# Optimization experiments

Hardware: AMD Instinct MI355X
Metric: run time of the kernel (lower is better)

The kernel has to match this reference:

```python
import jax, jax.numpy as jnp
import numpy as np

DEPTH = 16
Q_DIM = 64
V_DIM = 64
BATCH = 2048


def setup_inputs() -> dict:
    key = jax.random.key(0)
    k1, k2, k3 = jax.random.split(key, 3)
    query = jax.random.normal(k1, (BATCH, Q_DIM), dtype=jnp.float32)
    # internal-node keys: (2^depth - 1) nodes, each with 2 child keys of dim q_dim
    tree_key = jax.random.normal(k2, (2 ** DEPTH - 1, 2, Q_DIM), dtype=jnp.float32)
    # leaf values: 2^depth leaves of dim v_dim
    tree_value = jax.random.normal(k3, (2 ** DEPTH, V_DIM), dtype=jnp.float32)
    return {"query": query, "tree_key": tree_key, "tree_value": tree_value}


def _tree_attention(query, tree_key, tree_value, depth):
    # Hierarchical softmax attention over a complete binary tree.
    # At each internal node, a 2-way softmax over <query, child_key> logits
    # splits probability mass between left/right subtrees; leaf weight is the
    # product of probabilities along its root-to-leaf path.
    B = query.shape[0]
    probs = jnp.ones((B, 1), dtype=query.dtype)
    start = 0
    for d in range(depth):
        n = 2 ** d  # nodes at this level, stored contiguously at [start, start+n)
        level_keys = tree_key[start:start + n]           # (n, 2, q_dim)
        logits = jnp.einsum('bq,ncq->bnc', query, level_keys)  # (B, n, 2)
        p = jax.nn.softmax(logits, axis=-1)               # (B, n, 2)
        probs = (probs[:, :, None] * p).reshape(B, 2 * n)  # (B, 2n)
        start += n
    # weighted combination of leaf values: (B, 2^depth) @ (2^depth, v_dim)
    return probs @ tree_value


def reference(query, tree_key, tree_value):
    return _tree_attention(query, tree_key, tree_value, DEPTH)
```

## Files before the change

kernel.cpp:

```cpp
#include <hip/hip_runtime.h>

#define LOG2E 1.44269504088896f

typedef _Float16 half8  __attribute__((ext_vector_type(8)));
typedef _Float16 half4v __attribute__((ext_vector_type(4)));
typedef float    floatx4 __attribute__((ext_vector_type(4)));

#define WS_KD   0u
#define WS_VT   8388608u
#define WS_PART 16777216u

__device__ __forceinline__ floatx4 mfma16(half8 a, half8 b, floatx4 c) {
    return __builtin_amdgcn_mfma_f32_16x16x32_f16(a, b, c, 0, 0, 0);
}

__device__ __forceinline__ float sigmf(float d) {
    return __builtin_amdgcn_rcpf(1.0f + __builtin_amdgcn_exp2f(d * (-LOG2E)));
}

__device__ __forceinline__ void gl_lds16(const void* gsrc, void* ldst) {
    __builtin_amdgcn_global_load_lds(
        (const __attribute__((address_space(1))) unsigned int*)gsrc,
        (__attribute__((address_space(3))) unsigned int*)ldst,
        16, 0, 0);
}

__global__ __launch_bounds__(256)
void prep_kd(const float* __restrict__ tkey, char* __restrict__ ws)
{
    const int gt  = blockIdx.x * 256 + threadIdx.x;
    const int rid = gt >> 3, part = gt & 7;
    const int s = rid >> 6, j = rid & 63;
    const size_t dst = (size_t)WS_KD + (size_t)s * 8192 + j * 128 + ((part * 16) ^ ((j & 7) << 4));
    half8 out;
    if (j < 63) {
        const int u = j + 1;
        const int f = 31 - __builtin_clz(u);
        const int i = u - (1 << f);
        const int gidx = ((1 << (10 + f)) - 1) + (s << f) + i;
        const floatx4* kp = (const floatx4*)(tkey + (size_t)gidx * 128) + part * 2;
        floatx4 a0 = kp[0], a1 = kp[1];
        floatx4 b0 = kp[16], b1 = kp[17];
        #pragma unroll
        for (int e = 0; e < 4; ++e) {
            out[e]     = (_Float16)(a0[e] - b0[e]);
            out[4 + e] = (_Float16)(a1[e] - b1[e]);
        }
    } else {
        #pragma unroll
        for (int e = 0; e < 8; ++e) out[e] = (_Float16)0.f;
    }
    *(half8*)(ws + dst) = out;
}

__global__ __launch_bounds__(256)
void prep_vt(const float* __restrict__ tval, char* __restrict__ ws)
{
    __shared__ _Float16 sT[64 * 72];
    const int s = blockIdx.x, tid = threadIdx.x;
    {
        const int l = tid >> 2, part = tid & 3;
        const floatx4* vp = (const floatx4*)(tval + ((size_t)s * 64 + l) * 64) + part * 4;
        #pragma unroll
        for (int t4 = 0; t4 < 4; ++t4) {
            floatx4 f = vp[t4];
            #pragma unroll
            for (int e = 0; e < 4; ++e)
                sT[(part * 16 + t4 * 4 + e) * 72 + l] = (_Float16)f[e];
        }
    }
    __syncthreads();
    {
        const int v = tid >> 2, q4 = tid & 3;
        half8 x0 = *(const half8*)(sT + v * 72 + 16 * q4);
        half8 x1 = *(const half8*)(sT + v * 72 + 16 * q4 + 8);
        char* base = ws + WS_VT + (size_t)s * 8192 + v * 128;
        const int swz = (v & 7) << 4;
        *(half8*)(base + ((q4 * 32)      ^ swz)) = x0;
        *(half8*)(base + ((q4 * 32 + 16) ^ swz)) = x1;
    }
}

#define RD(n) ((float)sProb[(n) * 256 + (bb ^ (((n) & 7) << 3))])

__global__ __launch_bounds__(256, 2)
void tree_attn(const float* __restrict__ q,
               const float* __restrict__ tkey,
               const char* __restrict__ wsc,
               _Float16* __restrict__ pout)
{
    __shared__ _Float16 sA[256 * 72];
    __shared__ _Float16 sProb[64 * 256];
    __shared__ _Float16 sB[64 * 64];

    const int tid  = threadIdx.x;
    const int w    = tid >> 6;
    const int lane = tid & 63;
    const int lm   = lane & 15;
    const int quad = lane >> 4;
    const int xcd  = blockIdx.x & 7;
    const int ix   = blockIdx.x >> 3;
    const int g    = xcd * 8 + (ix >> 3);
    const int tb   = ix & 7;

    {
        const int j = tid >> 3, part = tid & 7;
        int gidx = -1;
        if (j < 6) {
            gidx = (1 << j) - 1 + (g >> (6 - j));
        } else if (j < 21) {
            const int u = j - 5;
            const int e = 31 - __builtin_clz(u);
            const int i = u - (1 << e);
            gidx = ((1 << (6 + e)) - 1) + (g << e) + i;
        }
        half8 out;
        if (gidx >= 0) {
            const floatx4* kp = (const floatx4*)(tkey + (size_t)gidx * 128) + part * 2;
            floatx4 a0 = kp[0], a1 = kp[1];
            floatx4 b0 = kp[16], b1 = kp[17];
            #pragma unroll
            for (int e = 0; e < 4; ++e) {
                out[e]     = (_Float16)(a0[e] - b0[e]);
                out[4 + e] = (_Float16)(a1[e] - b1[e]);
            }
        } else {
            #pragma unroll
            for (int e = 0; e < 8; ++e) out[e] = (_Float16)0.f;
        }
        *(half8*)(sB + j * 64 + ((part * 8) ^ ((j & 7) << 3))) = out;
    }

    {
        const int r = tid;
        const floatx4* qp = (const floatx4*)(q + (size_t)(tb * 256 + r) * 64);
        const int sw = (r & 7) << 3;
        #pragma unroll
        for (int t4 = 0; t4 < 8; ++t4) {
            floatx4 f0 = qp[2 * t4], f1 = qp[2 * t4 + 1];
            half8 hv;
            #pragma unroll
            for (int e = 0; e < 4; ++e) { hv[e] = (_Float16)f0[e]; hv[4 + e] = (_Float16)f1[e]; }
            *(half8*)(sA + r * 64 + ((t4 * 8) ^ sw)) = hv;
        }
    }
    __syncthreads();

    half8 qA[4][2];
    #pragma unroll
    for (int m = 0; m < 4; ++m) {
        const int rA = 64 * w + 16 * m + lm;
        const int sw = (lm & 7) << 3;
        #pragma unroll
        for (int kt = 0; kt < 2; ++kt)
            qA[m][kt] = *(const half8*)(sA + rA * 64 + ((kt * 32 + quad * 8) ^ sw));
    }

    {
        #pragma unroll
        for (int nt = 0; nt < 2; ++nt) {
            const int row = 16 * nt + lm;
            const int sw = (lm & 7) << 3;
            half8 bf0 = *(const half8*)(sB + row * 64 + ((quad * 8) ^ sw));
            half8 bf1 = *(const half8*)(sB + row * 64 + ((32 + quad * 8) ^ sw));
            floatx4 acc[4];
            #pragma unroll
            for (int m = 0; m < 4; ++m) {
                acc[m][0] = 0.f; acc[m][1] = 0.f; acc[m][2] = 0.f; acc[m][3] = 0.f;
                acc[m] = mfma16(qA[m][0], bf0, acc[m]);
                acc[m] = mfma16(qA[m][1], bf1, acc[m]);
            }
            #pragma unroll
            for (int m = 0; m < 4; ++m) {
                half4v ph;
                #pragma unroll
                for (int r = 0; r < 4; ++r) ph[r] = (_Float16)sigmf(acc[m][r]);
                const int col = 64 * w + 16 * m + 4 * quad;
                *(half4v*)(sProb + row * 256 + (col ^ sw)) = ph;
            }
        }
    }
    __syncthreads();

    const int bb = tid;
    float pref = 1.f;
    #pragma unroll
    for (int d = 0; d < 6; ++d) {
        float pv = RD(d);
        pref *= ((g >> (5 - d)) & 1) ? (1.f - pv) : pv;
    }
    const float p6   = RD(6);
    const float p7_0 = RD(7),  p7_1 = RD(8);
    const float p9_0 = RD(9),  p9_1 = RD(10), p9_2 = RD(11), p9_3 = RD(12);
    const float p13_0 = RD(13), p13_1 = RD(14), p13_2 = RD(15), p13_3 = RD(16);
    const float p13_4 = RD(17), p13_5 = RD(18), p13_6 = RD(19), p13_7 = RD(20);

    floatx4 O[4][4];
    #pragma unroll
    for (int m = 0; m < 4; ++m)
        #pragma unroll
        for (int nt = 0; nt < 4; ++nt) { O[m][nt][0]=0.f; O[m][nt][1]=0.f; O[m][nt][2]=0.f; O[m][nt][3]=0.f; }

    for (int sl = 0; sl < 16; ++sl) {
        const int s = (g << 4) + sl;

        {
            const char* kd = wsc + WS_KD + (size_t)s * 8192;
            gl_lds16(kd + w * 2048 +        lane * 16, sB + w * 1024);
            gl_lds16(kd + w * 2048 + 1024 + lane * 16, sB + w * 1024 + 512);
        }
        half8 vf[4][2];
        {
            const char* vt = wsc + WS_VT + (size_t)s * 8192;
            #pragma unroll
            for (int nt = 0; nt < 4; ++nt) {
                const int row = 16 * nt + lm;
                const int swz = (lm & 7) << 4;
                #pragma unroll
                for (int kt = 0; kt < 2; ++kt)
                    vf[nt][kt] = *(const half8*)(vt + row * 128 + ((kt * 64 + quad * 16) ^ swz));
            }
        }
        __syncthreads();

        __builtin_amdgcn_s_setprio(1);
        #pragma unroll
        for (int nt = 0; nt < 4; ++nt) {
            const int row = 16 * nt + lm;
            const int sw = (lm & 7) << 3;
            half8 bf0 = *(const half8*)(sB + row * 64 + ((quad * 8) ^ sw));
            half8 bf1 = *(const half8*)(sB + row * 64 + ((32 + quad * 8) ^ sw));
            floatx4 acc[4];
            #pragma unroll
            for (int m = 0; m < 4; ++m) {
                acc[m][0] = 0.f; acc[m][1] = 0.f; acc[m][2] = 0.f; acc[m][3] = 0.f;
                acc[m] = mfma16(qA[m][0], bf0, acc[m]);
                acc[m] = mfma16(qA[m][1], bf1, acc[m]);
            }
            #pragma unroll
            for (int m = 0; m < 4; ++m) {
                half4v ph;
                #pragma unroll
                for (int r = 0; r < 4; ++r) ph[r] = (_Float16)sigmf(acc[m][r]);
                const int col = 64 * w + 16 * m + 4 * quad;
                *(half4v*)(sProb + row * 256 + (col ^ sw)) = ph;
            }
        }
        __builtin_amdgcn_s_setprio(0);
        __syncthreads();

        const int a0 = sl >> 3, a1 = sl >> 2, a2 = sl >> 1;
        float P0v = pref * (a0 ? (1.f - p6) : p6);
        { float v7 = a0 ? p7_1 : p7_0;                    P0v *= (a1 & 1) ? (1.f - v7) : v7; }
        { float v9 = (a1 == 0) ? p9_0 : (a1 == 1) ? p9_1 : (a1 == 2) ? p9_2 : p9_3;
                                                          P0v *= (a2 & 1) ? (1.f - v9) : v9; }
        { float vd = (a2 == 0) ? p13_0 : (a2 == 1) ? p13_1 : (a2 == 2) ? p13_2 : (a2 == 3) ? p13_3
                   : (a2 == 4) ? p13_4 : (a2 == 5) ? p13_5 : (a2 == 6) ? p13_6 : p13_7;
                                                          P0v *= (sl & 1) ? (1.f - vd) : vd; }

        {
            #pragma unroll
            for (int qq = 0; qq < 4; ++qq) {
                float p0 = RD(0);
                float p1 = RD(1 + (qq >> 1));
                float P2 = P0v * (((qq >> 1) & 1) ? (1.f - p0) : p0)
                               * ((qq & 1) ? (1.f - p1) : p1);
                float p2 = RD(3 + qq);
                float A3[2]; A3[0] = P2 * p2; A3[1] = P2 * (1.f - p2);
                float A4[4];
                #pragma unroll
                for (int c = 0; c < 2; ++c) {
                    float pv = RD(7 + 2 * qq + c);
                    A4[2 * c] = A3[c] * pv; A4[2 * c + 1] = A3[c] * (1.f - pv);
                }
                float A5[8];
                #pragma unroll
                for (int n = 0; n < 4; ++n) {
                    float pv = RD(15 + 4 * qq + n);
                    A5[2 * n] = A4[n] * pv; A5[2 * n + 1] = A4[n] * (1.f - pv);
                }
                half8 lo, hi;
                #pragma unroll
                for (int n = 0; n < 8; ++n) {
                    float pv = RD(31 + 8 * qq + n);
                    float e0 = A5[n] * pv;
                    float e1 = A5[n] * (1.f - pv);
                    if (n < 4) { lo[2 * n] = (_Float16)e0; lo[2 * n + 1] = (_Float16)e1; }
                    else       { hi[2 * (n - 4)] = (_Float16)e0; hi[2 * (n - 4) + 1] = (_Float16)e1; }
                }
                const int sw = (bb & 7) << 3;
                *(half8*)(sA + bb * 64 + ((16 * qq)     ^ sw)) = lo;
                *(half8*)(sA + bb * 64 + ((16 * qq + 8) ^ sw)) = hi;
            }
        }
        __syncthreads();

        {
            half8 af[4][2];
            #pragma unroll
            for (int m = 0; m < 4; ++m) {
                const int rA = 64 * w + 16 * m + lm;
                const int sw = (lm & 7) << 3;
                #pragma unroll
                for (int kt = 0; kt < 2; ++kt)
                    af[m][kt] = *(const half8*)(sA + rA * 64 + ((kt * 32 + quad * 8) ^ sw));
            }
            __builtin_amdgcn_s_setprio(1);
            #pragma unroll
            for (int nt = 0; nt < 4; ++nt)
                #pragma unroll
                for (int kt = 0; kt < 2; ++kt) {
                    O[0][nt] = mfma16(af[0][kt], vf[nt][kt], O[0][nt]);
                    O[1][nt] = mfma16(af[1][kt], vf[nt][kt], O[1][nt]);
                    O[2][nt] = mfma16(af[2][kt], vf[nt][kt], O[2][nt]);
                    O[3][nt] = mfma16(af[3][kt], vf[nt][kt], O[3][nt]);
                }
            __builtin_amdgcn_s_setprio(0);
        }
    }

    __syncthreads();
    #pragma unroll
    for (int m = 0; m < 4; ++m)
        #pragma unroll
        for (int nt = 0; nt < 4; ++nt)
            #pragma unroll
            for (int r = 0; r < 4; ++r)
                sA[(64 * w + 16 * m + 4 * quad + r) * 72 + 16 * nt + lm] = (_Float16)O[m][nt][r];
    __syncthreads();
    {
        const int row = tid;
        _Float16* dst = pout + ((size_t)g * 2048 + tb * 256 + row) * 64;
        #pragma unroll
        for (int j = 0; j < 8; ++j)
            *(half8*)(dst + j * 8) = *(const half8*)(sA + row * 72 + j * 8);
    }
}

__global__ __launch_bounds__(256)
void tree_reduce(const _Float16* __restrict__ part, float* __restrict__ outp)
{
    const int idx = blockIdx.x * 256 + threadIdx.x;
    float s[8];
    #pragma unroll
    for (int e = 0; e < 8; ++e) s[e] = 0.f;
    for (int gg = 0; gg < 64; ++gg) {
        half8 v = *(const half8*)(part + (size_t)gg * 131072 + (size_t)idx * 8);
        #pragma unroll
        for (int e = 0; e < 8; ++e) s[e] += (float)v[e];
    }
    floatx4 o0, o1;
    #pragma unroll
    for (int e = 0; e < 4; ++e) { o0[e] = s[e]; o1[e] = s[4 + e]; }
    float* dst = outp + (size_t)idx * 8;
    *(floatx4*)dst = o0;
    *(floatx4*)(dst + 4) = o1;
}

extern "C" void kernel_launch(void* const* d_in, const int* in_sizes, int n_in,
                              void* d_out, int out_size, void* d_ws, size_t ws_size,
                              hipStream_t stream)
{
    const float* q  = (const float*)d_in[0];
    const float* tk = (const float*)d_in[1];
    const float* tv = (const float*)d_in[2];
    float* outp = (float*)d_out;
    char*  ws   = (char*)d_ws;
    _Float16* partp = (_Float16*)(ws + WS_PART);

    prep_kd<<<dim3(2048), dim3(256), 0, stream>>>(tk, ws);
    prep_vt<<<dim3(1024), dim3(256), 0, stream>>>(tv, ws);
    tree_attn<<<dim3(512), dim3(256), 0, stream>>>(q, tk, ws, partp);
    tree_reduce<<<dim3(64), dim3(256), 0, stream>>>(partp, outp);
}
```

Before: 169.1 us.

## Merge prep kernels, transpose probability tile, vectorize prob reads, widen reduce grid

```diff
diff --git a/kernel.cpp b/kernel.cpp
--- a/kernel.cpp
+++ b/kernel.cpp
@@ -26,41 +26,15 @@
 }
 
 __global__ __launch_bounds__(256)
-void prep_kd(const float* __restrict__ tkey, char* __restrict__ ws)
-{
-    const int gt  = blockIdx.x * 256 + threadIdx.x;
-    const int rid = gt >> 3, part = gt & 7;
-    const int s = rid >> 6, j = rid & 63;
-    const size_t dst = (size_t)WS_KD + (size_t)s * 8192 + j * 128 + ((part * 16) ^ ((j & 7) << 4));
-    half8 out;
-    if (j < 63) {
-        const int u = j + 1;
-        const int f = 31 - __builtin_clz(u);
-        const int i = u - (1 << f);
-        const int gidx = ((1 << (10 + f)) - 1) + (s << f) + i;
-        const floatx4* kp = (const floatx4*)(tkey + (size_t)gidx * 128) + part * 2;
-        floatx4 a0 = kp[0], a1 = kp[1];
-        floatx4 b0 = kp[16], b1 = kp[17];
-        #pragma unroll
-        for (int e = 0; e < 4; ++e) {
-            out[e]     = (_Float16)(a0[e] - b0[e]);
-            out[4 + e] = (_Float16)(a1[e] - b1[e]);
-        }
-    } else {
-        #pragma unroll
-        for (int e = 0; e < 8; ++e) out[e] = (_Float16)0.f;
-    }
-    *(half8*)(ws + dst) = out;
-}
-
-__global__ __launch_bounds__(256)
-void prep_vt(const float* __restrict__ tval, char* __restrict__ ws)
+void k_prep(const float* __restrict__ tkey, const float* __restrict__ tval,
+            char* __restrict__ ws)
 {
     __shared__ _Float16 sT[64 * 72];
-    const int s = blockIdx.x, tid = threadIdx.x;
+    const int bid = blockIdx.x, tid = threadIdx.x;
+
     {
         const int l = tid >> 2, part = tid & 3;
-        const floatx4* vp = (const floatx4*)(tval + ((size_t)s * 64 + l) * 64) + part * 4;
+        const floatx4* vp = (const floatx4*)(tval + ((size_t)bid * 64 + l) * 64) + part * 4;
         #pragma unroll
         for (int t4 = 0; t4 < 4; ++t4) {
             floatx4 f = vp[t4];
@@ -74,23 +48,48 @@
         const int v = tid >> 2, q4 = tid & 3;
         half8 x0 = *(const half8*)(sT + v * 72 + 16 * q4);
         half8 x1 = *(const half8*)(sT + v * 72 + 16 * q4 + 8);
-        char* base = ws + WS_VT + (size_t)s * 8192 + v * 128;
+        char* base = ws + WS_VT + (size_t)bid * 8192 + v * 128;
         const int swz = (v & 7) << 4;
         *(half8*)(base + ((q4 * 32)      ^ swz)) = x0;
         *(half8*)(base + ((q4 * 32 + 16) ^ swz)) = x1;
     }
-}
-
-#define RD(n) ((float)sProb[(n) * 256 + (bb ^ (((n) & 7) << 3))])
+
+    #pragma unroll
+    for (int k = 0; k < 2; ++k) {
+        const int gt  = bid * 512 + k * 256 + tid;
+        const int rid = gt >> 3, part = gt & 7;
+        const int s = rid >> 6, j = rid & 63;
+        const size_t dst = (size_t)WS_KD + (size_t)s * 8192 + j * 128 + ((part * 16) ^ ((j & 7) << 4));
+        half8 out;
+        if (j < 63) {
+            const int u = j + 1;
+            const int f = 31 - __builtin_clz(u);
+            const int i = u - (1 << f);
+            const int gidx = ((1 << (10 + f)) - 1) + (s << f) + i;
+            const floatx4* kp = (const floatx4*)(tkey + (size_t)gidx * 128) + part * 2;
+            floatx4 a0 = kp[0], a1 = kp[1];
+            floatx4 b0 = kp[16], b1 = kp[17];
+            #pragma unroll
+            for (int e = 0; e < 4; ++e) {
+                out[e]     = (_Float16)(a0[e] - b0[e]);
+                out[4 + e] = (_Float16)(a1[e] - b1[e]);
+            }
+        } else {
+            #pragma unroll
+            for (int e = 0; e < 8; ++e) out[e] = (_Float16)0.f;
+        }
+        *(half8*)(ws + dst) = out;
+    }
+}
 
 __global__ __launch_bounds__(256, 2)
-void tree_attn(const float* __restrict__ q,
-               const float* __restrict__ tkey,
-               const char* __restrict__ wsc,
-               _Float16* __restrict__ pout)
+void k_main(const float* __restrict__ q,
+            const float* __restrict__ tkey,
+            const char* __restrict__ wsc,
+            _Float16* __restrict__ pout)
 {
-    __shared__ _Float16 sA[256 * 72];
-    __shared__ _Float16 sProb[64 * 256];
+    __shared__ _Float16 sA[256 * 64];
+    __shared__ _Float16 sPT[256 * 72];
     __shared__ _Float16 sB[64 * 64];
 
     const int tid  = threadIdx.x;
@@ -167,16 +166,15 @@
             #pragma unroll
             for (int m = 0; m < 4; ++m) {
                 acc[m][0] = 0.f; acc[m][1] = 0.f; acc[m][2] = 0.f; acc[m][3] = 0.f;
-                acc[m] = mfma16(qA[m][0], bf0, acc[m]);
-                acc[m] = mfma16(qA[m][1], bf1, acc[m]);
+                acc[m] = mfma16(bf0, qA[m][0], acc[m]);
+                acc[m] = mfma16(bf1, qA[m][1], acc[m]);
             }
             #pragma unroll
             for (int m = 0; m < 4; ++m) {
                 half4v ph;
                 #pragma unroll
                 for (int r = 0; r < 4; ++r) ph[r] = (_Float16)sigmf(acc[m][r]);
-                const int col = 64 * w + 16 * m + 4 * quad;
-                *(half4v*)(sProb + row * 256 + (col ^ sw)) = ph;
+                *(half4v*)(sPT + (64 * w + 16 * m + lm) * 72 + 16 * nt + 4 * quad) = ph;
             }
         }
     }
@@ -186,14 +184,17 @@
     float pref = 1.f;
     #pragma unroll
     for (int d = 0; d < 6; ++d) {
-        float pv = RD(d);
+        float pv = (float)sPT[bb * 72 + d];
         pref *= ((g >> (5 - d)) & 1) ? (1.f - pv) : pv;
     }
-    const float p6   = RD(6);
-    const float p7_0 = RD(7),  p7_1 = RD(8);
-    const float p9_0 = RD(9),  p9_1 = RD(10), p9_2 = RD(11), p9_3 = RD(12);
-    const float p13_0 = RD(13), p13_1 = RD(14), p13_2 = RD(15), p13_3 = RD(16);
-    const float p13_4 = RD(17), p13_5 = RD(18), p13_6 = RD(19), p13_7 = RD(20);
+    const float p6    = (float)sPT[bb * 72 + 6];
+    const float p7_0  = (float)sPT[bb * 72 + 7],  p7_1  = (float)sPT[bb * 72 + 8];
+    const float p9_0  = (float)sPT[bb * 72 + 9],  p9_1  = (float)sPT[bb * 72 + 10];
+    const float p9_2  = (float)sPT[bb * 72 + 11], p9_3  = (float)sPT[bb * 72 + 12];
+    const float p13_0 = (float)sPT[bb * 72 + 13], p13_1 = (float)sPT[bb * 72 + 14];
+    const float p13_2 = (float)sPT[bb * 72 + 15], p13_3 = (float)sPT[bb * 72 + 16];
+    const float p13_4 = (float)sPT[bb * 72 + 17], p13_5 = (float)sPT[bb * 72 + 18];
+    const float p13_6 = (float)sPT[bb * 72 + 19], p13_7 = (float)sPT[bb * 72 + 20];
 
     floatx4 O[4][4];
     #pragma unroll
@@ -234,16 +235,15 @@
             #pragma unroll
             for (int m = 0; m < 4; ++m) {
                 acc[m][0] = 0.f; acc[m][1] = 0.f; acc[m][2] = 0.f; acc[m][3] = 0.f;
-                acc[m] = mfma16(qA[m][0], bf0, acc[m]);
-                acc[m] = mfma16(qA[m][1], bf1, acc[m]);
+                acc[m] = mfma16(bf0, qA[m][0], acc[m]);
+                acc[m] = mfma16(bf1, qA[m][1], acc[m]);
             }
             #pragma unroll
             for (int m = 0; m < 4; ++m) {
                 half4v ph;
                 #pragma unroll
                 for (int r = 0; r < 4; ++r) ph[r] = (_Float16)sigmf(acc[m][r]);
-                const int col = 64 * w + 16 * m + 4 * quad;
-                *(half4v*)(sProb + row * 256 + (col ^ sw)) = ph;
+                *(half4v*)(sPT + (64 * w + 16 * m + lm) * 72 + 16 * nt + 4 * quad) = ph;
             }
         }
         __builtin_amdgcn_s_setprio(0);
@@ -258,31 +258,37 @@
                    : (a2 == 4) ? p13_4 : (a2 == 5) ? p13_5 : (a2 == 6) ? p13_6 : p13_7;
                                                           P0v *= (sl & 1) ? (1.f - vd) : vd; }
 
+        half8 pr[8];
+        #pragma unroll
+        for (int t = 0; t < 8; ++t)
+            pr[t] = *(const half8*)(sPT + bb * 72 + t * 8);
+        #define PN(n) ((float)pr[(n) >> 3][(n) & 7])
+
         {
             #pragma unroll
             for (int qq = 0; qq < 4; ++qq) {
-                float p0 = RD(0);
-                float p1 = RD(1 + (qq >> 1));
+                float p0 = PN(0);
+                float p1 = PN(1 + (qq >> 1));
                 float P2 = P0v * (((qq >> 1) & 1) ? (1.f - p0) : p0)
                                * ((qq & 1) ? (1.f - p1) : p1);
-                float p2 = RD(3 + qq);
+                float p2 = PN(3 + qq);
                 float A3[2]; A3[0] = P2 * p2; A3[1] = P2 * (1.f - p2);
                 float A4[4];
                 #pragma unroll
                 for (int c = 0; c < 2; ++c) {
-                    float pv = RD(7 + 2 * qq + c);
+                    float pv = PN(7 + 2 * qq + c);
                     A4[2 * c] = A3[c] * pv; A4[2 * c + 1] = A3[c] * (1.f - pv);
                 }
                 float A5[8];
                 #pragma unroll
                 for (int n = 0; n < 4; ++n) {
-                    float pv = RD(15 + 4 * qq + n);
+                    float pv = PN(15 + 4 * qq + n);
                     A5[2 * n] = A4[n] * pv; A5[2 * n + 1] = A4[n] * (1.f - pv);
                 }
                 half8 lo, hi;
                 #pragma unroll
                 for (int n = 0; n < 8; ++n) {
-                    float pv = RD(31 + 8 * qq + n);
+                    float pv = PN(31 + 8 * qq + n);
                     float e0 = A5[n] * pv;
                     float e1 = A5[n] * (1.f - pv);
                     if (n < 4) { lo[2 * n] = (_Float16)e0; lo[2 * n + 1] = (_Float16)e1; }
@@ -293,6 +299,7 @@
                 *(half8*)(sA + bb * 64 + ((16 * qq + 8) ^ sw)) = hi;
             }
         }
+        #undef PN
         __syncthreads();
 
         {
@@ -325,36 +332,34 @@
         #pragma unroll
         for (int nt = 0; nt < 4; ++nt)
             #pragma unroll
-            for (int r = 0; r < 4; ++r)
-                sA[(64 * w + 16 * m + 4 * quad + r) * 72 + 16 * nt + lm] = (_Float16)O[m][nt][r];
+            for (int r = 0; r < 4; ++r) {
+                const int row = 64 * w + 16 * m + 4 * quad + r;
+                const int col = 16 * nt + lm;
+                sA[row * 64 + (col ^ ((row & 7) << 3))] = (_Float16)O[m][nt][r];
+            }
     __syncthreads();
     {
         const int row = tid;
         _Float16* dst = pout + ((size_t)g * 2048 + tb * 256 + row) * 64;
+        const int sw = (row & 7) << 3;
         #pragma unroll
         for (int j = 0; j < 8; ++j)
-            *(half8*)(dst + j * 8) = *(const half8*)(sA + row * 72 + j * 8);
+            *(half8*)(dst + j * 8) = *(const half8*)(sA + row * 64 + ((j * 8) ^ sw));
     }
 }
 
 __global__ __launch_bounds__(256)
-void tree_reduce(const _Float16* __restrict__ part, float* __restrict__ outp)
+void k_reduce(const _Float16* __restrict__ part, float* __restrict__ outp)
 {
     const int idx = blockIdx.x * 256 + threadIdx.x;
-    float s[8];
-    #pragma unroll
-    for (int e = 0; e < 8; ++e) s[e] = 0.f;
+    float s0 = 0.f, s1 = 0.f, s2 = 0.f, s3 = 0.f;
+    #pragma unroll 8
     for (int gg = 0; gg < 64; ++gg) {
-        half8 v = *(const half8*)(part + (size_t)gg * 131072 + (size_t)idx * 8);
-        #pragma unroll
-        for (int e = 0; e < 8; ++e) s[e] += (float)v[e];
-    }
-    floatx4 o0, o1;
-    #pragma unroll
-    for (int e = 0; e < 4; ++e) { o0[e] = s[e]; o1[e] = s[4 + e]; }
-    float* dst = outp + (size_t)idx * 8;
-    *(floatx4*)dst = o0;
-    *(floatx4*)(dst + 4) = o1;
+        half4v v = *(const half4v*)(part + (size_t)gg * 131072 + (size_t)idx * 4);
+        s0 += (float)v[0]; s1 += (float)v[1]; s2 += (float)v[2]; s3 += (float)v[3];
+    }
+    floatx4 o; o[0] = s0; o[1] = s1; o[2] = s2; o[3] = s3;
+    *(floatx4*)(outp + (size_t)idx * 4) = o;
 }
 
 extern "C" void kernel_launch(void* const* d_in, const int* in_sizes, int n_in,
@@ -368,8 +373,7 @@
     char*  ws   = (char*)d_ws;
     _Float16* partp = (_Float16*)(ws + WS_PART);
 
-    prep_kd<<<dim3(2048), dim3(256), 0, stream>>>(tk, ws);
-    prep_vt<<<dim3(1024), dim3(256), 0, stream>>>(tv, ws);
-    tree_attn<<<dim3(512), dim3(256), 0, stream>>>(q, tk, ws, partp);
-    tree_reduce<<<dim3(64), dim3(256), 0, stream>>>(partp, outp);
-}
+    k_prep  <<<dim3(1024), dim3(256), 0, stream>>>(tk, tv, ws);
+    k_main  <<<dim3(512),  dim3(256), 0, stream>>>(q, tk, ws, partp);
+    k_reduce<<<dim3(128),  dim3(256), 0, stream>>>(partp, outp);
+}
```

New measurement: 166.1 us. Within noise of the previous version (-1.7%).
